# Kernel tuning notes

Hardware: AMD Instinct MI355X
Metric: run time of the kernel (lower is better)

## Reference

```python
import jax, jax.numpy as jnp
import numpy as np

DIM = 768
HEADS = 12
SCALE = DIM ** -0.5  # NOTE: module scales by full dim, not head dim


def setup_inputs() -> dict:
    key = jax.random.key(0)
    ks = jax.random.split(key, 5)
    B, N, C = 8, 1024, DIM
    x = jax.random.normal(ks[0], (B, N, C), dtype=jnp.float32)
    W_qkv = jax.random.normal(ks[1], (C, 3 * C), dtype=jnp.float32) * (C ** -0.5)
    b_qkv = jnp.zeros((3 * C,), dtype=jnp.float32)
    W_out = jax.random.normal(ks[2], (C, C), dtype=jnp.float32) * (C ** -0.5)
    b_out = jnp.zeros((C,), dtype=jnp.float32)
    return {"x": x, "W_qkv": W_qkv, "b_qkv": b_qkv, "W_out": W_out, "b_out": b_out}


def reference(x, W_qkv, b_qkv, W_out, b_out) -> jnp.ndarray:
    B, N, C = x.shape
    H, D = HEADS, C // HEADS
    qkv = x @ W_qkv + b_qkv                       # [B, N, 3C]
    q, k, v = jnp.split(qkv, 3, axis=-1)
    # [B, N, C] -> [B, H, N, D]
    q = q.reshape(B, N, H, D).transpose(0, 2, 1, 3)
    k = k.reshape(B, N, H, D).transpose(0, 2, 1, 3)
    v = v.reshape(B, N, H, D).transpose(0, 2, 1, 3)
    attn = jnp.einsum("bhnd,bhmd->bhnm", q, k) * SCALE
    attn = jax.nn.softmax(attn, axis=-1)
    out = jnp.einsum("bhnm,bhmd->bhnd", attn, v)   # [B, H, N, D]
    out = out.transpose(0, 2, 1, 3).reshape(B, N, C)
    return out @ W_out + b_out
```

## Files before the change

kernel.cpp:

```cpp
#include <hip/hip_runtime.h>
#include <hip/hip_bf16.h>

typedef __attribute__((ext_vector_type(4))) float f32x4;
typedef __attribute__((ext_vector_type(4))) unsigned u32x4;
typedef __attribute__((ext_vector_type(8))) short bf16x8;

#define SCALE_F 0.03608439182435161f
#define QSCALE  (0.03608439182435161f * 1.44269504088896f)

__device__ __forceinline__ unsigned short f2bf(float f) {
    union { float f; unsigned u; } v; v.f = f;
    return (unsigned short)((v.u + 0x7FFFu + ((v.u >> 16) & 1u)) >> 16);
}

__device__ __forceinline__ float fast_exp2(float x) {
#if __has_builtin(__builtin_amdgcn_exp2f)
    return __builtin_amdgcn_exp2f(x);
#else
    return exp2f(x);
#endif
}

__device__ __forceinline__ void gload_lds16(const void* g, void* l) {
    __builtin_amdgcn_global_load_lds(
        (const __attribute__((address_space(1))) unsigned int*)g,
        (__attribute__((address_space(3))) unsigned int*)l, 16, 0, 0);
}

__global__ __launch_bounds__(256) void xcvt_kernel(const float* __restrict__ X,
                                                   unsigned short* __restrict__ Xb,
                                                   int n8) {
    const int i = blockIdx.x * 256 + threadIdx.x;
    if (i < n8) {
        f32x4 a = *(const f32x4*)(X + (size_t)i * 8);
        f32x4 b = *(const f32x4*)(X + (size_t)i * 8 + 4);
        bf16x8 w;
#pragma unroll
        for (int j = 0; j < 4; ++j) { w[j] = (short)f2bf(a[j]); w[4 + j] = (short)f2bf(b[j]); }
        *(bf16x8*)(Xb + (size_t)i * 8) = w;
    }
}

__global__ __launch_bounds__(256) void wtrans_kernel(const float* __restrict__ W,
                                                     unsigned short* __restrict__ WT,
                                                     int R, int C) {
    __shared__ unsigned short T[64][68];
    const int t = threadIdx.x;
    const int r0 = blockIdx.y * 64, c0 = blockIdx.x * 64;
    {
        const int lr = t >> 4, lc = (t & 15) * 4;
#pragma unroll
        for (int p = 0; p < 4; ++p) {
            const float* s = W + (size_t)(r0 + lr + p * 16) * C + c0 + lc;
            f32x4 v = *(const f32x4*)s;
            unsigned short* d = &T[lr + p * 16][lc];
            d[0] = f2bf(v[0]); d[1] = f2bf(v[1]); d[2] = f2bf(v[2]); d[3] = f2bf(v[3]);
        }
    }
    __syncthreads();
    {
        const int oc = t >> 3, j0 = (t & 7) * 8;
#pragma unroll
        for (int p = 0; p < 2; ++p) {
            const int c = oc + p * 32;
            bf16x8 v;
#pragma unroll
            for (int j = 0; j < 8; ++j) v[j] = (short)T[j0 + j][c];
            *(bf16x8*)(WT + (size_t)(c0 + c) * R + r0 + j0) = v;
        }
    }
}

__global__ __launch_bounds__(256) void qkv_gemm_kernel(
    const unsigned short* __restrict__ Xb, const unsigned short* __restrict__ WT,
    const float* __restrict__ bias,
    unsigned short* __restrict__ Qw, unsigned short* __restrict__ Kw,
    unsigned short* __restrict__ VTw)
{
    __shared__ unsigned short Alds[128 * 32];
    __shared__ unsigned short Blds[128 * 32];

    const int t = threadIdx.x;
    const int lane = t & 63, wave = t >> 6;
    const int l15 = lane & 15, l4 = lane >> 4;
    const int m0 = blockIdx.x * 128, n0 = blockIdx.y * 128;
    const int wr = wave >> 1, wc = wave & 1;

    f32x4 acc[4][4];
#pragma unroll
    for (int m = 0; m < 4; ++m)
#pragma unroll
        for (int n = 0; n < 4; ++n) acc[m][n] = (f32x4){0.f, 0.f, 0.f, 0.f};

    for (int k0 = 0; k0 < 768; k0 += 32) {
#pragma unroll
        for (int c = 0; c < 2; ++c) {
            const int o = wave * 1024 + lane * 16 + c * 4096;
            const int row = o >> 6, cb = o & 63;
            gload_lds16((const char*)(Xb + (size_t)(m0 + row) * 768 + k0) + cb,
                        (char*)Alds + wave * 1024 + c * 4096);
            gload_lds16((const char*)(WT + (size_t)(n0 + row) * 768 + k0) + cb,
                        (char*)Blds + wave * 1024 + c * 4096);
        }
        __syncthreads();
        bf16x8 af[4], bfr[4];
#pragma unroll
        for (int m = 0; m < 4; ++m)
            af[m] = *(const bf16x8*)((const char*)Alds + (wr * 64 + m * 16 + l15) * 64 + l4 * 16);
#pragma unroll
        for (int n = 0; n < 4; ++n)
            bfr[n] = *(const bf16x8*)((const char*)Blds + (wc * 64 + n * 16 + l15) * 64 + l4 * 16);
#pragma unroll
        for (int m = 0; m < 4; ++m)
#pragma unroll
            for (int n = 0; n < 4; ++n)
                acc[m][n] = __builtin_amdgcn_mfma_f32_16x16x32_bf16(af[m], bfr[n], acc[m][n], 0, 0, 0);
        __syncthreads();
    }

#pragma unroll
    for (int n = 0; n < 4; ++n) {
        const int col = n0 + wc * 64 + n * 16 + l15;
        const float bv = bias[col];
        const int which = col / 768;
        const int cc = col - which * 768;
        const int h = cc >> 6, dd = cc & 63;
#pragma unroll
        for (int m = 0; m < 4; ++m) {
#pragma unroll
            for (int r = 0; r < 4; ++r) {
                const int row = m0 + wr * 64 + m * 16 + l4 * 4 + r;
                const int b = row >> 10, ntok = row & 1023;
                const size_t bh = (size_t)b * 12 + h;
                float val = acc[m][n][r] + bv;
                if (which == 0) val *= QSCALE;
                const unsigned short hv = f2bf(val);
                if (which == 0)      Qw[(bh * 1024 + ntok) * 64 + dd] = hv;
                else if (which == 1) Kw[(bh * 1024 + ntok) * 64 + dd] = hv;
                else                 VTw[(bh * 64 + dd) * 1024 + ntok] = hv;
            }
        }
    }
}

__global__ __launch_bounds__(256) void attn_kernel(
    const unsigned short* __restrict__ Qw, const unsigned short* __restrict__ Kw,
    const unsigned short* __restrict__ VTw, unsigned short* __restrict__ A2)
{
    __shared__ unsigned short Klds[2 * 64 * 64];
    __shared__ unsigned short Vlds[2 * 64 * 64];
    __shared__ float Flds[4 * 16];

    const int t = threadIdx.x, lane = t & 63, wave = t >> 6;
    const int l15 = lane & 15, l4 = lane >> 4;
    const int wg = (blockIdx.x & 7) * 192 + (blockIdx.x >> 3);
    const int qt = wg & 15, bh = wg >> 4;
    const int q0 = qt * 64;

    const size_t kvbase = (size_t)bh * 1024 * 64;
    const size_t vtbase = (size_t)bh * 64 * 1024;

    const unsigned short* qptr = Qw + kvbase + (size_t)(q0 + wave * 16 + l15) * 64;
    const bf16x8 qf0 = *(const bf16x8*)((const char*)qptr + l4 * 16);
    const bf16x8 qf1 = *(const bf16x8*)((const char*)qptr + 64 + l4 * 16);

    f32x4 oacc[4];
#pragma unroll
    for (int d = 0; d < 4; ++d) oacc[d] = (f32x4){0.f, 0.f, 0.f, 0.f};
    float m_run = -1e30f, l_run = 0.f;

    auto STAGE = [&](int kt, int bufi) {
        const int kv0 = kt * 64;
        char* kb = (char*)Klds + bufi * 8192;
        char* vb = (char*)Vlds + bufi * 8192;
#pragma unroll
        for (int c = 0; c < 2; ++c) {
            const int oo = wave * 1024 + lane * 16 + c * 4096;
            const int R = oo >> 7, w = oo & 127;
            const int sw = w ^ ((R & 7) << 4);
            const int kvs = (R & 0x23) | ((R & 0x0C) << 1) | ((R & 0x10) >> 2);
            gload_lds16((const char*)(Kw + kvbase + (size_t)(kv0 + kvs) * 64) + sw,
                        kb + wave * 1024 + c * 4096);
            gload_lds16((const char*)(VTw + vtbase + (size_t)R * 1024 + kv0) + sw,
                        vb + wave * 1024 + c * 4096);
        }
    };

    STAGE(0, 0);
    for (int kt = 0; kt < 16; ++kt) {
        const int cur = kt & 1;
        if (kt < 15) {
            STAGE(kt + 1, cur ^ 1);
            asm volatile("s_waitcnt vmcnt(4)" ::: "memory");
        } else {
            asm volatile("s_waitcnt vmcnt(0)" ::: "memory");
        }
        __builtin_amdgcn_s_barrier();
        __builtin_amdgcn_sched_barrier(0);
        const char* kb = (const char*)Klds + cur * 8192;
        const char* vb = (const char*)Vlds + cur * 8192;

        f32x4 sacc[4];
#pragma unroll
        for (int i = 0; i < 4; ++i) sacc[i] = (f32x4){0.f, 0.f, 0.f, 0.f};
        __builtin_amdgcn_s_setprio(1);
#pragma unroll
        for (int ks = 0; ks < 2; ++ks) {
            const bf16x8 qq = ks ? qf1 : qf0;
#pragma unroll
            for (int kvf = 0; kvf < 4; ++kvf) {
                const int row = kvf * 16 + l15;
                int addr = row * 128 + ks * 64 + l4 * 16;
                addr ^= (row & 7) << 4;
                const bf16x8 kf = *(const bf16x8*)(kb + addr);
                sacc[kvf] = __builtin_amdgcn_mfma_f32_16x16x32_bf16(kf, qq, sacc[kvf], 0, 0, 0);
            }
        }
        __builtin_amdgcn_s_setprio(0);

        float p[16];
        float tmax = -1e30f;
#pragma unroll
        for (int i = 0; i < 4; ++i)
#pragma unroll
            for (int r = 0; r < 4; ++r) {
                p[i * 4 + r] = sacc[i][r];
                tmax = fmaxf(tmax, sacc[i][r]);
            }
        tmax = fmaxf(tmax, __shfl_xor(tmax, 16));
        tmax = fmaxf(tmax, __shfl_xor(tmax, 32));

        if (!__all(tmax - m_run <= 8.f)) {
            const float mnew = fmaxf(m_run, tmax);
            const float alpha = fast_exp2(m_run - mnew);
            m_run = mnew;
            if (lane < 16) Flds[wave * 16 + lane] = alpha;
            const f32x4 av = *(const f32x4*)(&Flds[wave * 16 + l4 * 4]);
#pragma unroll
            for (int d = 0; d < 4; ++d)
#pragma unroll
                for (int r = 0; r < 4; ++r) oacc[d][r] *= av[r];
            l_run *= alpha;
        }

        float tsum = 0.f;
#pragma unroll
        for (int i = 0; i < 16; ++i) { p[i] = fast_exp2(p[i] - m_run); tsum += p[i]; }
        tsum += __shfl_xor(tsum, 16);
        tsum += __shfl_xor(tsum, 32);
        l_run += tsum;

        bf16x8 paf[2];
#pragma unroll
        for (int ks = 0; ks < 2; ++ks) {
            union { u32x4 u; bf16x8 h; } cv;
#pragma unroll
            for (int j2 = 0; j2 < 4; ++j2)
                asm("v_cvt_pk_bf16_f32 %0, %1, %2"
                    : "=v"(cv.u[j2]) : "v"(p[ks * 8 + 2 * j2]), "v"(p[ks * 8 + 2 * j2 + 1]));
            paf[ks] = cv.h;
        }

        __builtin_amdgcn_s_setprio(1);
#pragma unroll
        for (int ks = 0; ks < 2; ++ks) {
#pragma unroll
            for (int df = 0; df < 4; ++df) {
                const int d = df * 16 + l15;
                int addr = d * 128 + ks * 64 + l4 * 16;
                addr ^= (d & 7) << 4;
                const bf16x8 vf = *(const bf16x8*)(vb + addr);
                oacc[df] = __builtin_amdgcn_mfma_f32_16x16x32_bf16(paf[ks], vf, oacc[df], 0, 0, 0);
            }
        }
        __builtin_amdgcn_s_setprio(0);
        __builtin_amdgcn_s_barrier();
    }

    if (lane < 16) Flds[wave * 16 + lane] = 1.f / l_run;
    const f32x4 inv = *(const f32x4*)(&Flds[wave * 16 + l4 * 4]);
    const int b = bh / 12, h = bh - b * 12;
#pragma unroll
    for (int df = 0; df < 4; ++df) {
#pragma unroll
        for (int r = 0; r < 4; ++r) {
            const int row = b * 1024 + q0 + wave * 16 + l4 * 4 + r;
            const int col = h * 64 + df * 16 + l15;
            A2[(size_t)row * 768 + col] = f2bf(oacc[df][r] * inv[r]);
        }
    }
}

__global__ __launch_bounds__(256) void out_gemm_kernel(
    const unsigned short* __restrict__ A2, const unsigned short* __restrict__ WT,
    const float* __restrict__ bias, float* __restrict__ Out)
{
    __shared__ unsigned short Alds[128 * 32];
    __shared__ unsigned short Blds[128 * 32];

    const int t = threadIdx.x;
    const int lane = t & 63, wave = t >> 6;
    const int l15 = lane & 15, l4 = lane >> 4;
    const int m0 = blockIdx.x * 128, n0 = blockIdx.y * 128;
    const int wr = wave >> 1, wc = wave & 1;

    f32x4 acc[4][4];
#pragma unroll
    for (int m = 0; m < 4; ++m)
#pragma unroll
        for (int n = 0; n < 4; ++n) acc[m][n] = (f32x4){0.f, 0.f, 0.f, 0.f};

    for (int k0 = 0; k0 < 768; k0 += 32) {
#pragma unroll
        for (int c = 0; c < 2; ++c) {
            const int o = wave * 1024 + lane * 16 + c * 4096;
            const int row = o >> 6, cb = o & 63;
            gload_lds16((const char*)(A2 + (size_t)(m0 + row) * 768 + k0) + cb,
                        (char*)Alds + wave * 1024 + c * 4096);
            gload_lds16((const char*)(WT + (size_t)(n0 + row) * 768 + k0) + cb,
                        (char*)Blds + wave * 1024 + c * 4096);
        }
        __syncthreads();
        bf16x8 af[4], bfr[4];
#pragma unroll
        for (int m = 0; m < 4; ++m)
            af[m] = *(const bf16x8*)((const char*)Alds + (wr * 64 + m * 16 + l15) * 64 + l4 * 16);
#pragma unroll
        for (int n = 0; n < 4; ++n)
            bfr[n] = *(const bf16x8*)((const char*)Blds + (wc * 64 + n * 16 + l15) * 64 + l4 * 16);
#pragma unroll
        for (int m = 0; m < 4; ++m)
#pragma unroll
            for (int n = 0; n < 4; ++n)
                acc[m][n] = __builtin_amdgcn_mfma_f32_16x16x32_bf16(af[m], bfr[n], acc[m][n], 0, 0, 0);
        __syncthreads();
    }

#pragma unroll
    for (int n = 0; n < 4; ++n) {
        const int col = n0 + wc * 64 + n * 16 + l15;
        const float bv = bias[col];
#pragma unroll
        for (int m = 0; m < 4; ++m)
#pragma unroll
            for (int r = 0; r < 4; ++r) {
                const int row = m0 + wr * 64 + m * 16 + l4 * 4 + r;
                Out[(size_t)row * 768 + col] = acc[m][n][r] + bv;
            }
    }
}

extern "C" void kernel_launch(void* const* d_in, const int* in_sizes, int n_in,
                              void* d_out, int out_size, void* d_ws, size_t ws_size,
                              hipStream_t stream) {
    const float* X    = (const float*)d_in[0];
    const float* Wqkv = (const float*)d_in[1];
    const float* bqkv = (const float*)d_in[2];
    const float* Wout = (const float*)d_in[3];
    const float* bout = (const float*)d_in[4];
    float* Out = (float*)d_out;

    const size_t nq = (size_t)96 * 1024 * 64;
    unsigned short* XbA2  = (unsigned short*)d_ws;
    unsigned short* Qw    = XbA2 + nq;
    unsigned short* Kw    = Qw + nq;
    unsigned short* VTw   = Kw + nq;
    unsigned short* WqkvT = VTw + nq;
    unsigned short* WoutT = WqkvT + (size_t)2304 * 768;

    hipLaunchKernelGGL(xcvt_kernel, dim3(3072), dim3(256), 0, stream,
                       X, XbA2, 8192 * 768 / 8);
    hipLaunchKernelGGL(wtrans_kernel, dim3(36, 12), dim3(256), 0, stream,
                       Wqkv, WqkvT, 768, 2304);
    hipLaunchKernelGGL(wtrans_kernel, dim3(12, 12), dim3(256), 0, stream,
                       Wout, WoutT, 768, 768);
    hipLaunchKernelGGL(qkv_gemm_kernel, dim3(64, 18), dim3(256), 0, stream,
                       XbA2, WqkvT, bqkv, Qw, Kw, VTw);
    hipLaunchKernelGGL(attn_kernel, dim3(1536), dim3(256), 0, stream,
                       Qw, Kw, VTw, XbA2);
    hipLaunchKernelGGL(out_gemm_kernel, dim3(64, 6), dim3(256), 0, stream,
                       XbA2, WoutT, bout, Out);
}
```

Baseline: 138.8 us.

## Double-buffer LDS tiles with XOR swizzle in QKV and output GEMMs

Both GEMM kernels now keep two LDS stages. The next K-tile is fetched with global_load_lds while the current tile feeds the MFMAs, and explicit vmcnt waits plus raw s_barrier replace the two syncthreads per iteration. The LDS layout XOR-swizzles the 16-byte column chunk by row to reduce bank conflicts on the fragment reads. Wave priority is raised around the MFMA block. LDS use doubles, which may cut occupancy, and the hand-written waitcnt/barrier ordering risks race conditions if the compiler reorders memory operations.

Result: slower. 142.4 us (+2.6%).

```diff
diff --git a/kernel.cpp b/kernel.cpp
--- a/kernel.cpp
+++ b/kernel.cpp
@@ -77,8 +77,8 @@
     unsigned short* __restrict__ Qw, unsigned short* __restrict__ Kw,
     unsigned short* __restrict__ VTw)
 {
-    __shared__ unsigned short Alds[128 * 32];
-    __shared__ unsigned short Blds[128 * 32];
+    __shared__ unsigned short Alds[2][128 * 32];
+    __shared__ unsigned short Blds[2][128 * 32];
 
     const int t = threadIdx.x;
     const int lane = t & 63, wave = t >> 6;
@@ -92,30 +92,52 @@
 #pragma unroll
         for (int n = 0; n < 4; ++n) acc[m][n] = (f32x4){0.f, 0.f, 0.f, 0.f};
 
-    for (int k0 = 0; k0 < 768; k0 += 32) {
+    auto STAGE = [&](int k0, int bufi) {
 #pragma unroll
         for (int c = 0; c < 2; ++c) {
-            const int o = wave * 1024 + lane * 16 + c * 4096;
-            const int row = o >> 6, cb = o & 63;
-            gload_lds16((const char*)(Xb + (size_t)(m0 + row) * 768 + k0) + cb,
-                        (char*)Alds + wave * 1024 + c * 4096);
-            gload_lds16((const char*)(WT + (size_t)(n0 + row) * 768 + k0) + cb,
-                        (char*)Blds + wave * 1024 + c * 4096);
-        }
-        __syncthreads();
+            const int o = wave * 1024 + c * 4096 + lane * 16;
+            const int row = o >> 6;
+            const int kb = (o & 63) ^ ((row & 3) << 4);
+            gload_lds16((const char*)(Xb + (size_t)(m0 + row) * 768 + k0) + kb,
+                        (char*)&Alds[bufi][0] + wave * 1024 + c * 4096);
+            gload_lds16((const char*)(WT + (size_t)(n0 + row) * 768 + k0) + kb,
+                        (char*)&Blds[bufi][0] + wave * 1024 + c * 4096);
+        }
+    };
+
+    STAGE(0, 0);
+    for (int kt = 0; kt < 24; ++kt) {
+        const int cur = kt & 1;
+        if (kt < 23) {
+            STAGE((kt + 1) * 32, cur ^ 1);
+            asm volatile("s_waitcnt vmcnt(4)" ::: "memory");
+        } else {
+            asm volatile("s_waitcnt vmcnt(0)" ::: "memory");
+        }
+        __builtin_amdgcn_s_barrier();
+        __builtin_amdgcn_sched_barrier(0);
+
         bf16x8 af[4], bfr[4];
 #pragma unroll
-        for (int m = 0; m < 4; ++m)
-            af[m] = *(const bf16x8*)((const char*)Alds + (wr * 64 + m * 16 + l15) * 64 + l4 * 16);
-#pragma unroll
-        for (int n = 0; n < 4; ++n)
-            bfr[n] = *(const bf16x8*)((const char*)Blds + (wc * 64 + n * 16 + l15) * 64 + l4 * 16);
+        for (int m = 0; m < 4; ++m) {
+            const int row = wr * 64 + m * 16 + l15;
+            const int kb = (l4 * 16) ^ ((row & 3) << 4);
+            af[m] = *(const bf16x8*)((const char*)&Alds[cur][0] + row * 64 + kb);
+        }
+#pragma unroll
+        for (int n = 0; n < 4; ++n) {
+            const int row = wc * 64 + n * 16 + l15;
+            const int kb = (l4 * 16) ^ ((row & 3) << 4);
+            bfr[n] = *(const bf16x8*)((const char*)&Blds[cur][0] + row * 64 + kb);
+        }
+        __builtin_amdgcn_s_setprio(1);
 #pragma unroll
         for (int m = 0; m < 4; ++m)
 #pragma unroll
             for (int n = 0; n < 4; ++n)
                 acc[m][n] = __builtin_amdgcn_mfma_f32_16x16x32_bf16(af[m], bfr[n], acc[m][n], 0, 0, 0);
-        __syncthreads();
+        __builtin_amdgcn_s_setprio(0);
+        __builtin_amdgcn_s_barrier();
     }
 
 #pragma unroll
@@ -295,8 +317,8 @@
     const unsigned short* __restrict__ A2, const unsigned short* __restrict__ WT,
     const float* __restrict__ bias, float* __restrict__ Out)
 {
-    __shared__ unsigned short Alds[128 * 32];
-    __shared__ unsigned short Blds[128 * 32];
+    __shared__ unsigned short Alds[2][128 * 32];
+    __shared__ unsigned short Blds[2][128 * 32];
 
     const int t = threadIdx.x;
     const int lane = t & 63, wave = t >> 6;
@@ -310,30 +332,52 @@
 #pragma unroll
         for (int n = 0; n < 4; ++n) acc[m][n] = (f32x4){0.f, 0.f, 0.f, 0.f};
 
-    for (int k0 = 0; k0 < 768; k0 += 32) {
+    auto STAGE = [&](int k0, int bufi) {
 #pragma unroll
         for (int c = 0; c < 2; ++c) {
-            const int o = wave * 1024 + lane * 16 + c * 4096;
-            const int row = o >> 6, cb = o & 63;
-            gload_lds16((const char*)(A2 + (size_t)(m0 + row) * 768 + k0) + cb,
-                        (char*)Alds + wave * 1024 + c * 4096);
-            gload_lds16((const char*)(WT + (size_t)(n0 + row) * 768 + k0) + cb,
-                        (char*)Blds + wave * 1024 + c * 4096);
-        }
-        __syncthreads();
+            const int o = wave * 1024 + c * 4096 + lane * 16;
+            const int row = o >> 6;
+            const int kb = (o & 63) ^ ((row & 3) << 4);
+            gload_lds16((const char*)(A2 + (size_t)(m0 + row) * 768 + k0) + kb,
+                        (char*)&Alds[bufi][0] + wave * 1024 + c * 4096);
+            gload_lds16((const char*)(WT + (size_t)(n0 + row) * 768 + k0) + kb,
+                        (char*)&Blds[bufi][0] + wave * 1024 + c * 4096);
+        }
+    };
+
+    STAGE(0, 0);
+    for (int kt = 0; kt < 24; ++kt) {
+        const int cur = kt & 1;
+        if (kt < 23) {
+            STAGE((kt + 1) * 32, cur ^ 1);
+            asm volatile("s_waitcnt vmcnt(4)" ::: "memory");
+        } else {
+            asm volatile("s_waitcnt vmcnt(0)" ::: "memory");
+        }
+        __builtin_amdgcn_s_barrier();
+        __builtin_amdgcn_sched_barrier(0);
+
         bf16x8 af[4], bfr[4];
 #pragma unroll
-        for (int m = 0; m < 4; ++m)
-            af[m] = *(const bf16x8*)((const char*)Alds + (wr * 64 + m * 16 + l15) * 64 + l4 * 16);
-#pragma unroll
-        for (int n = 0; n < 4; ++n)
-            bfr[n] = *(const bf16x8*)((const char*)Blds + (wc * 64 + n * 16 + l15) * 64 + l4 * 16);
+        for (int m = 0; m < 4; ++m) {
+            const int row = wr * 64 + m * 16 + l15;
+            const int kb = (l4 * 16) ^ ((row & 3) << 4);
+            af[m] = *(const bf16x8*)((const char*)&Alds[cur][0] + row * 64 + kb);
+        }
+#pragma unroll
+        for (int n = 0; n < 4; ++n) {
+            const int row = wc * 64 + n * 16 + l15;
+            const int kb = (l4 * 16) ^ ((row & 3) << 4);
+            bfr[n] = *(const bf16x8*)((const char*)&Blds[cur][0] + row * 64 + kb);
+        }
+        __builtin_amdgcn_s_setprio(1);
 #pragma unroll
         for (int m = 0; m < 4; ++m)
 #pragma unroll
             for (int n = 0; n < 4; ++n)
                 acc[m][n] = __builtin_amdgcn_mfma_f32_16x16x32_bf16(af[m], bfr[n], acc[m][n], 0, 0, 0);
-        __syncthreads();
+        __builtin_amdgcn_s_setprio(0);
+        __builtin_amdgcn_s_barrier();
     }
 
 #pragma unroll
```

## Load V fragments straight to registers and shrink out-GEMM N tile

Applied to the files above, without the earlier changes.

In the attention kernel, V^T fragments are now read from global memory directly into registers each iteration instead of being staged through LDS. K moves to a triple-buffered LDS ring, which lets the trailing barrier be dropped, and the vmcnt waits are adjusted for the extra in-flight loads. Separately, the output GEMM tile narrows from 128x128 to 128x64, doubling the grid so more workgroups fill the CUs. The risks are uncoalesced or latency-exposed global loads for V, higher register pressure, and reduced A-tile reuse in the output GEMM.

New measurement: 185.3 us. 33.5% more time.

```diff
diff --git a/kernel.cpp b/kernel.cpp
--- a/kernel.cpp
+++ b/kernel.cpp
@@ -147,8 +147,7 @@
     const unsigned short* __restrict__ Qw, const unsigned short* __restrict__ Kw,
     const unsigned short* __restrict__ VTw, unsigned short* __restrict__ A2)
 {
-    __shared__ unsigned short Klds[2 * 64 * 64];
-    __shared__ unsigned short Vlds[2 * 64 * 64];
+    __shared__ unsigned short Klds[3 * 64 * 64];
     __shared__ float Flds[4 * 16];
 
     const int t = threadIdx.x, lane = t & 63, wave = t >> 6;
@@ -164,15 +163,16 @@
     const bf16x8 qf0 = *(const bf16x8*)((const char*)qptr + l4 * 16);
     const bf16x8 qf1 = *(const bf16x8*)((const char*)qptr + 64 + l4 * 16);
 
+    const unsigned short* vlane = VTw + vtbase + (size_t)l15 * 1024 + l4 * 8;
+
     f32x4 oacc[4];
 #pragma unroll
     for (int d = 0; d < 4; ++d) oacc[d] = (f32x4){0.f, 0.f, 0.f, 0.f};
     float m_run = -1e30f, l_run = 0.f;
 
-    auto STAGE = [&](int kt, int bufi) {
+    auto STAGE_K = [&](int kt, int bufi) {
         const int kv0 = kt * 64;
         char* kb = (char*)Klds + bufi * 8192;
-        char* vb = (char*)Vlds + bufi * 8192;
 #pragma unroll
         for (int c = 0; c < 2; ++c) {
             const int oo = wave * 1024 + lane * 16 + c * 4096;
@@ -181,24 +181,28 @@
             const int kvs = (R & 0x23) | ((R & 0x0C) << 1) | ((R & 0x10) >> 2);
             gload_lds16((const char*)(Kw + kvbase + (size_t)(kv0 + kvs) * 64) + sw,
                         kb + wave * 1024 + c * 4096);
-            gload_lds16((const char*)(VTw + vtbase + (size_t)R * 1024 + kv0) + sw,
-                        vb + wave * 1024 + c * 4096);
         }
     };
 
-    STAGE(0, 0);
+    STAGE_K(0, 0);
     for (int kt = 0; kt < 16; ++kt) {
-        const int cur = kt & 1;
+        bf16x8 vf[2][4];
+#pragma unroll
+        for (int ks = 0; ks < 2; ++ks)
+#pragma unroll
+            for (int df = 0; df < 4; ++df)
+                vf[ks][df] = *(const bf16x8*)(vlane + df * 16384 + kt * 64 + ks * 32);
         if (kt < 15) {
-            STAGE(kt + 1, cur ^ 1);
-            asm volatile("s_waitcnt vmcnt(4)" ::: "memory");
+            STAGE_K(kt + 1, (kt + 1) % 3);
+            __builtin_amdgcn_sched_barrier(0);
+            asm volatile("s_waitcnt vmcnt(10)" ::: "memory");
         } else {
-            asm volatile("s_waitcnt vmcnt(0)" ::: "memory");
+            __builtin_amdgcn_sched_barrier(0);
+            asm volatile("s_waitcnt vmcnt(8)" ::: "memory");
         }
         __builtin_amdgcn_s_barrier();
         __builtin_amdgcn_sched_barrier(0);
-        const char* kb = (const char*)Klds + cur * 8192;
-        const char* vb = (const char*)Vlds + cur * 8192;
+        const char* kb = (const char*)Klds + (kt % 3) * 8192;
 
         f32x4 sacc[4];
 #pragma unroll
@@ -263,18 +267,11 @@
 
         __builtin_amdgcn_s_setprio(1);
 #pragma unroll
-        for (int ks = 0; ks < 2; ++ks) {
-#pragma unroll
-            for (int df = 0; df < 4; ++df) {
-                const int d = df * 16 + l15;
-                int addr = d * 128 + ks * 64 + l4 * 16;
-                addr ^= (d & 7) << 4;
-                const bf16x8 vf = *(const bf16x8*)(vb + addr);
-                oacc[df] = __builtin_amdgcn_mfma_f32_16x16x32_bf16(paf[ks], vf, oacc[df], 0, 0, 0);
-            }
-        }
+        for (int ks = 0; ks < 2; ++ks)
+#pragma unroll
+            for (int df = 0; df < 4; ++df)
+                oacc[df] = __builtin_amdgcn_mfma_f32_16x16x32_bf16(paf[ks], vf[ks][df], oacc[df], 0, 0, 0);
         __builtin_amdgcn_s_setprio(0);
-        __builtin_amdgcn_s_barrier();
     }
 
     if (lane < 16) Flds[wave * 16 + lane] = 1.f / l_run;
@@ -296,19 +293,19 @@
     const float* __restrict__ bias, float* __restrict__ Out)
 {
     __shared__ unsigned short Alds[128 * 32];
-    __shared__ unsigned short Blds[128 * 32];
+    __shared__ unsigned short Blds[64 * 32];
 
     const int t = threadIdx.x;
     const int lane = t & 63, wave = t >> 6;
     const int l15 = lane & 15, l4 = lane >> 4;
-    const int m0 = blockIdx.x * 128, n0 = blockIdx.y * 128;
+    const int m0 = blockIdx.x * 128, n0 = blockIdx.y * 64;
     const int wr = wave >> 1, wc = wave & 1;
 
-    f32x4 acc[4][4];
+    f32x4 acc[4][2];
 #pragma unroll
     for (int m = 0; m < 4; ++m)
 #pragma unroll
-        for (int n = 0; n < 4; ++n) acc[m][n] = (f32x4){0.f, 0.f, 0.f, 0.f};
+        for (int n = 0; n < 2; ++n) acc[m][n] = (f32x4){0.f, 0.f, 0.f, 0.f};
 
     for (int k0 = 0; k0 < 768; k0 += 32) {
 #pragma unroll
@@ -317,28 +314,32 @@
             const int row = o >> 6, cb = o & 63;
             gload_lds16((const char*)(A2 + (size_t)(m0 + row) * 768 + k0) + cb,
                         (char*)Alds + wave * 1024 + c * 4096);
+        }
+        {
+            const int o = t * 16;
+            const int row = o >> 6, cb = o & 63;
             gload_lds16((const char*)(WT + (size_t)(n0 + row) * 768 + k0) + cb,
-                        (char*)Blds + wave * 1024 + c * 4096);
+                        (char*)Blds + o);
         }
         __syncthreads();
-        bf16x8 af[4], bfr[4];
+        bf16x8 af[4], bfr[2];
 #pragma unroll
         for (int m = 0; m < 4; ++m)
             af[m] = *(const bf16x8*)((const char*)Alds + (wr * 64 + m * 16 + l15) * 64 + l4 * 16);
 #pragma unroll
-        for (int n = 0; n < 4; ++n)
-            bfr[n] = *(const bf16x8*)((const char*)Blds + (wc * 64 + n * 16 + l15) * 64 + l4 * 16);
-#pragma unroll
-        for (int m = 0; m < 4; ++m)
-#pragma unroll
-            for (int n = 0; n < 4; ++n)
+        for (int n = 0; n < 2; ++n)
+            bfr[n] = *(const bf16x8*)((const char*)Blds + (wc * 32 + n * 16 + l15) * 64 + l4 * 16);
+#pragma unroll
+        for (int m = 0; m < 4; ++m)
+#pragma unroll
+            for (int n = 0; n < 2; ++n)
                 acc[m][n] = __builtin_amdgcn_mfma_f32_16x16x32_bf16(af[m], bfr[n], acc[m][n], 0, 0, 0);
         __syncthreads();
     }
 
 #pragma unroll
-    for (int n = 0; n < 4; ++n) {
-        const int col = n0 + wc * 64 + n * 16 + l15;
+    for (int n = 0; n < 2; ++n) {
+        const int col = n0 + wc * 32 + n * 16 + l15;
         const float bv = bias[col];
 #pragma unroll
         for (int m = 0; m < 4; ++m)
@@ -378,6 +379,6 @@
                        XbA2, WqkvT, bqkv, Qw, Kw, VTw);
     hipLaunchKernelGGL(attn_kernel, dim3(1536), dim3(256), 0, stream,
                        Qw, Kw, VTw, XbA2);
-    hipLaunchKernelGGL(out_gemm_kernel, dim3(64, 6), dim3(256), 0, stream,
+    hipLaunchKernelGGL(out_gemm_kernel, dim3(64, 12), dim3(256), 0, stream,
                        XbA2, WoutT, bout, Out);
 }
```
